# Kernel optimization log

Measured on AMD Instinct MI355X. Metric: run time of the kernel, lower is better.

## Reference

```python
import jax, jax.numpy as jnp
import numpy as np


def _pairwise_dist(x, y):
    # x: [b, n, d], y: [b, n, d] -> squared L2 distances [b, n, n]
    xx = jnp.sum(x * x, axis=-1)  # [b, n]
    yy = jnp.sum(y * y, axis=-1)  # [b, n]
    zz = jnp.einsum('bnd,bmd->bnm', x, y)  # [b, n, n]
    return xx[:, :, None] + yy[:, None, :] - 2.0 * zz


def setup_inputs() -> dict:
    key = jax.random.key(0)
    k1, k2 = jax.random.split(key)
    bs, n, d = 4, 8192, 3
    x = jax.random.normal(k1, (bs, n, d), dtype=jnp.float32)
    y = jax.random.normal(k2, (bs, n, d), dtype=jnp.float32)
    return {"x": x, "y": y}


def reference(x, y):
    bs, n_points, _ = x.shape
    dist1 = jnp.sqrt(_pairwise_dist(x, y))  # [b, n, n]
    values1 = jnp.min(dist1, axis=2)        # [b, n] min over y for each x point
    dist2 = jnp.sqrt(_pairwise_dist(y, x))
    values2 = jnp.min(dist2, axis=2)        # min over x for each y point
    a = jnp.sum(values1, axis=1) / n_points
    b = jnp.sum(values2, axis=1) / n_points
    return jnp.sum(a) / bs + jnp.sum(b) / bs
```

## Files before the change

kernel.cpp:

```cpp
#include <hip/hip_runtime.h>
#include <stdint.h>

typedef _Float16 half8 __attribute__((ext_vector_type(8)));
typedef float f32x16 __attribute__((ext_vector_type(16)));

#define NPTS 8192
#define BS 4
#define TOTQ 65536
#define TPB 256
#define NS 4
#define QPB 512
#define NCHUNK 4

#define AS1 __attribute__((address_space(1)))
#define AS3 __attribute__((address_space(3)))

__device__ __forceinline__ float4 f4min(float4 a, float4 b) {
    return make_float4(fminf(a.x, b.x), fminf(a.y, b.y), fminf(a.z, b.z), fminf(a.w, b.w));
}


__global__ __launch_bounds__(TPB) void pack_mfma_kernel(const float* __restrict__ x,
                                                        const float* __restrict__ y,
                                                        ushort* __restrict__ Afrag,
                                                        ushort* __restrict__ Bfrag,
                                                        float* __restrict__ nq) {
    int pid = blockIdx.x * TPB + threadIdx.x;
    const float* src = (pid < BS * NPTS) ? x : y;
    int idx = pid & (BS * NPTS - 1);
    float p0 = src[idx * 3 + 0], p1 = src[idx * 3 + 1], p2 = src[idx * 3 + 2];
    float nt = p0 * p0 + p1 * p1 + p2 * p2;

    _Float16 h0 = (_Float16)p0, h1 = (_Float16)p1, h2 = (_Float16)p2;
    _Float16 l0 = (_Float16)(p0 - (float)h0);
    _Float16 l1 = (_Float16)(p1 - (float)h1);
    _Float16 l2 = (_Float16)(p2 - (float)h2);
    _Float16 nh = (_Float16)nt;
    _Float16 nl = (_Float16)(nt - (float)nh);
    _Float16 t2 = (_Float16)-2.0f;
    _Float16 m0 = t2 * h0, m1 = t2 * h1, m2 = t2 * h2;
    _Float16 n0 = t2 * l0, n1 = t2 * l1, n2 = t2 * l2;
    _Float16 one = (_Float16)1.0f, zz = (_Float16)0.0f;

    half8 ag0 = {m0, m1, m2, n0, n1, n2, m0, m1};
    half8 ag1 = {m2, one, one, n0, n1, n2, zz, zz};
    half8 bg0 = {h0, h1, h2, h0, h1, h2, l0, l1};
    half8 bg1 = {l2, nh, nl, l0, l1, l2, zz, zz};

    int qid = pid;
    int tid2 = pid ^ (BS * NPTS);
    size_t ab = (size_t)(qid >> 5) * 512 + (size_t)(qid & 31) * 8;
    *(half8*)(Afrag + ab)       = ag0;
    *(half8*)(Afrag + ab + 256) = ag1;
    size_t bb = (size_t)(tid2 >> 5) * 512 + (size_t)(tid2 & 31) * 8;
    *(half8*)(Bfrag + bb)       = bg0;
    *(half8*)(Bfrag + bb + 256) = bg1;
    nq[qid] = nt;
}

__global__ __launch_bounds__(TPB, 2) void mfma_min_kernel(const ushort* __restrict__ Afrag,
                                                          const ushort* __restrict__ Bfrag,
                                                          float* __restrict__ partial) {
    __shared__ __align__(16) char lds[2][16384];
    const int tid = threadIdx.x;
    const int wave = tid >> 6;
    const int l = tid & 63;
    const int chunkid = blockIdx.x / NS;
    const int s = blockIdx.x % NS;
    const int qbase = chunkid * QPB;
    const int dir = qbase >> 15;
    const int b = (qbase >> 13) & 3;
    const int tbase = dir * (BS * NPTS) + b * NPTS + s * (NPTS / NS);

    half8 afr0, afr1, afr2, afr3;
    {
        const ushort* Aw = Afrag + ((size_t)(qbase >> 5) + wave * 4) * 512 + (size_t)l * 8;
        afr0 = *(const half8*)(Aw);
        afr1 = *(const half8*)(Aw + 512);
        afr2 = *(const half8*)(Aw + 1024);
        afr3 = *(const half8*)(Aw + 1536);
    }
    f32x16 mrun0, mrun1, mrun2, mrun3, zc;
#pragma unroll
    for (int r = 0; r < 16; ++r) {
        mrun0[r] = 3.4e38f; mrun1[r] = 3.4e38f;
        mrun2[r] = 3.4e38f; mrun3[r] = 3.4e38f;
        zc[r] = 0.0f;
    }

    const char* gB = (const char*)Bfrag + (size_t)(tbase >> 5) * 1024;

#define STAGE(buf, c)                                                                       \
    {                                                                                       \
        _Pragma("unroll")                                                                   \
        for (int i = 0; i < 4; ++i)                                                         \
            __builtin_amdgcn_global_load_lds(                                               \
                (const AS1 uint32_t*)(gB + (size_t)(c) * 16384 + i * 4096 + tid * 16),      \
                (AS3 uint32_t*)(&lds[buf][i * 4096 + wave * 1024]), 16, 0, 0);              \
    }

#define AGROUP(AF, MR, BB0, BB1)                                                            \
    {                                                                                       \
        f32x16 d0 = __builtin_amdgcn_mfma_f32_32x32x16_f16(AF, BB0, zc, 0, 0, 0);           \
        f32x16 d1 = __builtin_amdgcn_mfma_f32_32x32x16_f16(AF, BB1, zc, 0, 0, 0);           \
        _Pragma("unroll")                                                                   \
        for (int r = 0; r < 16; ++r)                                                        \
            MR[r] = fminf(fminf(MR[r], d0[r]), d1[r]);                                      \
        __builtin_amdgcn_sched_barrier(0);                                                  \
    }

#define COMPUTE(BB0, BB1)                                                                   \
    AGROUP(afr0, mrun0, BB0, BB1)                                                           \
    AGROUP(afr1, mrun1, BB0, BB1)                                                           \
    AGROUP(afr2, mrun2, BB0, BB1)                                                           \
    AGROUP(afr3, mrun3, BB0, BB1)

    STAGE(0, 0);
    __syncthreads();

    int cur = 0;
#pragma unroll 1
    for (int c = 0; c < NCHUNK; ++c) {
        if (c + 1 < NCHUNK) STAGE(cur ^ 1, c + 1);
        const char* B = lds[cur];
        half8 bA0 = *(const half8*)(B + l * 16);
        half8 bA1 = *(const half8*)(B + 1024 + l * 16);
        half8 bB0, bB1;
#pragma unroll 1
        for (int p = 0; p < 8; p += 2) {
            bB0 = *(const half8*)(B + (p + 1) * 2048 + l * 16);
            bB1 = *(const half8*)(B + (p + 1) * 2048 + 1024 + l * 16);
            COMPUTE(bA0, bA1);
            int pn = (p + 2) & 7;
            bA0 = *(const half8*)(B + pn * 2048 + l * 16);
            bA1 = *(const half8*)(B + pn * 2048 + 1024 + l * 16);
            COMPUTE(bB0, bB1);
        }
        if (c + 1 < NCHUNK) {
            __syncthreads();
            cur ^= 1;
        }
    }
#undef STAGE
#undef COMPUTE
#undef AGROUP

    __syncthreads();
    float* ep = (float*)(&lds[0][0]);
    const int hi4 = (l >> 5) * 4;
    const int col = l & 31;

#define EPASS(AA, MR)                                                                       \
    {                                                                                       \
        _Pragma("unroll")                                                                   \
        for (int r = 0; r < 16; ++r) {                                                      \
            int row = (r & 3) + 8 * (r >> 2) + hi4;                                         \
            ep[wave * 1152 + row * 36 + col] = MR[r];                                       \
        }                                                                                   \
    }                                                                                       \
    __syncthreads();                                                                        \
    if (tid < 128) {                                                                        \
        const float4* rp = (const float4*)(ep + (tid >> 5) * 1152 + (tid & 31) * 36);       \
        float4 a01 = f4min(rp[0], rp[1]), a23 = f4min(rp[2], rp[3]);                        \
        float4 a45 = f4min(rp[4], rp[5]), a67 = f4min(rp[6], rp[7]);                        \
        float4 t = f4min(f4min(a01, a23), f4min(a45, a67));                                 \
        float m = fminf(fminf(t.x, t.y), fminf(t.z, t.w));                                  \
        partial[(size_t)s * TOTQ + qbase + (tid >> 5) * 128 + (AA) * 32 + (tid & 31)] = m;  \
    }                                                                                       \
    __syncthreads();

    EPASS(0, mrun0)
    EPASS(1, mrun1)
    EPASS(2, mrun2)
    EPASS(3, mrun3)
#undef EPASS
}

__global__ __launch_bounds__(TPB) void combine_mfma_kernel(const float* __restrict__ partial,
                                                           const float* __restrict__ nq,
                                                           float* __restrict__ bsum) {
    int q = blockIdx.x * TPB + threadIdx.x;
    float m = partial[q];
#pragma unroll
    for (int s = 1; s < NS; ++s)
        m = fminf(m, partial[(size_t)s * TOTQ + q]);
    float d = sqrtf(fmaxf(m + nq[q], 0.0f));
    __shared__ float red[TPB];
    red[threadIdx.x] = d;
    __syncthreads();
    for (int off = TPB / 2; off > 0; off >>= 1) {
        if (threadIdx.x < off) red[threadIdx.x] += red[threadIdx.x + off];
        __syncthreads();
    }
    if (threadIdx.x == 0) bsum[blockIdx.x] = red[0];
}

__global__ __launch_bounds__(TPB) void final_kernel(const float* __restrict__ bsum,
                                                    float* __restrict__ out) {
    __shared__ float red[TPB];
    red[threadIdx.x] = bsum[threadIdx.x];
    __syncthreads();
    for (int off = TPB / 2; off > 0; off >>= 1) {
        if (threadIdx.x < off) red[threadIdx.x] += red[threadIdx.x + off];
        __syncthreads();
    }
    if (threadIdx.x == 0) out[0] = red[0] * (1.0f / 32768.0f);
}

#define QPT 8
#define QPBF (TPB * QPT)
#define NGROUP (TOTQ / QPBF)
#define FNS 8

__global__ __launch_bounds__(TPB) void pack_kernel(const float* __restrict__ x,
                                                   const float* __restrict__ y,
                                                   float4* __restrict__ px,
                                                   float4* __restrict__ py) {
    int i = blockIdx.x * TPB + threadIdx.x;
    if (i < BS * NPTS) {
        float x0 = x[i * 3 + 0], x1 = x[i * 3 + 1], x2 = x[i * 3 + 2];
        px[i] = make_float4(x0, x1, x2, x0 * x0 + x1 * x1 + x2 * x2);
        float y0 = y[i * 3 + 0], y1 = y[i * 3 + 1], y2 = y[i * 3 + 2];
        py[i] = make_float4(y0, y1, y2, y0 * y0 + y1 * y1 + y2 * y2);
    }
}

__global__ __launch_bounds__(TPB) void chamfer_min_kernel(const float4* __restrict__ px,
                                                          const float4* __restrict__ py,
                                                          float* __restrict__ partial) {
    constexpr int SLICE = NPTS / FNS;
    __shared__ float4 tile[SLICE];
    const int t = threadIdx.x;
    const int g = blockIdx.x / FNS;
    const int s = blockIdx.x % FNS;
    const int dir = g >> 4;
    const int b = (g >> 2) & 3;
    const int chunk = g & 3;
    const float4* q  = (dir == 0 ? px : py) + b * NPTS + chunk * QPBF;
    const float4* tg = (dir == 0 ? py : px) + b * NPTS + s * SLICE;
    float a0[QPT], a1[QPT], a2[QPT], qq[QPT], mv[QPT];
#pragma unroll
    for (int i = 0; i < QPT; ++i) {
        float4 v = q[i * TPB + t];
        a0[i] = -2.0f * v.x; a1[i] = -2.0f * v.y; a2[i] = -2.0f * v.z;
        qq[i] = v.w; mv[i] = 3.4e38f;
    }
#pragma unroll
    for (int i = 0; i < SLICE / TPB; ++i)
        tile[i * TPB + t] = tg[i * TPB + t];
    __syncthreads();
#pragma unroll 2
    for (int j = 0; j < SLICE; j += 2) {
        float4 v0 = tile[j], v1 = tile[j + 1];
#pragma unroll
        for (int i = 0; i < QPT; ++i) {
            float d0 = fmaf(a2[i], v0.z, fmaf(a1[i], v0.y, fmaf(a0[i], v0.x, v0.w)));
            float d1 = fmaf(a2[i], v1.z, fmaf(a1[i], v1.y, fmaf(a0[i], v1.x, v1.w)));
            mv[i] = fminf(fminf(mv[i], d0), d1);
        }
    }
    const int qg0 = g * QPBF;
#pragma unroll
    for (int i = 0; i < QPT; ++i)
        partial[(size_t)s * TOTQ + qg0 + i * TPB + t] = mv[i] + qq[i];
}

__global__ __launch_bounds__(TPB) void combine_kernel(const float* __restrict__ partial,
                                                      float* __restrict__ bsum) {
    int idx = blockIdx.x * TPB + threadIdx.x;
    float m = 3.4e38f;
#pragma unroll
    for (int s = 0; s < FNS; ++s)
        m = fminf(m, partial[(size_t)s * TOTQ + idx]);
    float d = sqrtf(fmaxf(m, 0.0f));
    __shared__ float red[TPB];
    red[threadIdx.x] = d;
    __syncthreads();
    for (int off = TPB / 2; off > 0; off >>= 1) {
        if (threadIdx.x < off) red[threadIdx.x] += red[threadIdx.x + off];
        __syncthreads();
    }
    if (threadIdx.x == 0) bsum[blockIdx.x] = red[0];
}

extern "C" void kernel_launch(void* const* d_in, const int* in_sizes, int n_in,
                              void* d_out, int out_size, void* d_ws, size_t ws_size,
                              hipStream_t stream) {
    const float* x = (const float*)d_in[0];
    const float* y = (const float*)d_in[1];
    float* out = (float*)d_out;
    char* ws = (char*)d_ws;

    const size_t off_B = 2ull << 20;
    const size_t off_nq = 4ull << 20;
    const size_t off_pt = off_nq + (size_t)TOTQ * 4;
    const size_t off_bs = off_pt + (size_t)NS * TOTQ * 4;
    const size_t need = off_bs + 1024;

    if (ws_size >= need) {
        ushort* Afrag = (ushort*)ws;
        ushort* Bfrag = (ushort*)(ws + off_B);
        float* nq = (float*)(ws + off_nq);
        float* partial = (float*)(ws + off_pt);
        float* bsum = (float*)(ws + off_bs);
        hipLaunchKernelGGL(pack_mfma_kernel, dim3(TOTQ / TPB), dim3(TPB), 0, stream,
                           x, y, Afrag, Bfrag, nq);
        hipLaunchKernelGGL(mfma_min_kernel, dim3((TOTQ / QPB) * NS), dim3(TPB), 0, stream,
                           Afrag, Bfrag, partial);
        hipLaunchKernelGGL(combine_mfma_kernel, dim3(TOTQ / TPB), dim3(TPB), 0, stream,
                           partial, nq, bsum);
        hipLaunchKernelGGL(final_kernel, dim3(1), dim3(TPB), 0, stream, bsum, out);
    } else {
        float4* px = (float4*)ws;
        float4* py = (float4*)(ws + 512 * 1024);
        float* partial = (float*)(ws + 1024 * 1024);
        float* bsum = (float*)(ws + 1024 * 1024 + (size_t)FNS * TOTQ * 4);
        hipLaunchKernelGGL(pack_kernel, dim3((BS * NPTS + TPB - 1) / TPB), dim3(TPB), 0, stream,
                           x, y, px, py);
        hipLaunchKernelGGL(chamfer_min_kernel, dim3(NGROUP * FNS), dim3(TPB), 0, stream,
                           px, py, partial);
        hipLaunchKernelGGL(combine_kernel, dim3(TOTQ / TPB), dim3(TPB), 0, stream,
                           partial, bsum);
        hipLaunchKernelGGL(final_kernel, dim3(1), dim3(TPB), 0, stream, bsum, out);
    }
}
```

Measured before the change: 33.72 us.

## Fuse final reduction via last-block atomic counter and software-pipeline MFMA/min folds

The final single-block reduction kernel is folded into the combine kernel. A global atomic counter, reset in the pack kernel, lets the last block to finish sum the per-block partials, which removes one kernel launch. The MFMA inner loop is also reordered so each pair of MFMAs for the next A fragment is issued before the fminf fold of the previous results, with sched barriers placed to overlap matrix work with VALU min work. This costs extra accumulator registers, which may reduce occupancy, and adds an atomic and a release/acquire ordering step to the combine path.

```diff
diff --git a/kernel.cpp b/kernel.cpp
--- a/kernel.cpp
+++ b/kernel.cpp
@@ -24,8 +24,10 @@
                                                         const float* __restrict__ y,
                                                         ushort* __restrict__ Afrag,
                                                         ushort* __restrict__ Bfrag,
-                                                        float* __restrict__ nq) {
+                                                        float* __restrict__ nq,
+                                                        int* __restrict__ counter) {
     int pid = blockIdx.x * TPB + threadIdx.x;
+    if (pid == 0) *counter = 0;
     const float* src = (pid < BS * NPTS) ? x : y;
     int idx = pid & (BS * NPTS - 1);
     float p0 = src[idx * 3 + 0], p1 = src[idx * 3 + 1], p2 = src[idx * 3 + 2];
@@ -99,21 +101,34 @@
                 (AS3 uint32_t*)(&lds[buf][i * 4096 + wave * 1024]), 16, 0, 0);              \
     }
 
-#define AGROUP(AF, MR, BB0, BB1)                                                            \
+#define PAIR(AF, D0, D1, BB0, BB1)                                                          \
+    D0 = __builtin_amdgcn_mfma_f32_32x32x16_f16(AF, BB0, zc, 0, 0, 0);                      \
+    D1 = __builtin_amdgcn_mfma_f32_32x32x16_f16(AF, BB1, zc, 0, 0, 0);
+
+#define FOLD(MR, D0, D1)                                                                    \
     {                                                                                       \
-        f32x16 d0 = __builtin_amdgcn_mfma_f32_32x32x16_f16(AF, BB0, zc, 0, 0, 0);           \
-        f32x16 d1 = __builtin_amdgcn_mfma_f32_32x32x16_f16(AF, BB1, zc, 0, 0, 0);           \
         _Pragma("unroll")                                                                   \
         for (int r = 0; r < 16; ++r)                                                        \
-            MR[r] = fminf(fminf(MR[r], d0[r]), d1[r]);                                      \
-        __builtin_amdgcn_sched_barrier(0);                                                  \
+            MR[r] = fminf(fminf(MR[r], D0[r]), D1[r]);                          \
     }
 
 #define COMPUTE(BB0, BB1)                                                                   \
-    AGROUP(afr0, mrun0, BB0, BB1)                                                           \
-    AGROUP(afr1, mrun1, BB0, BB1)                                                           \
-    AGROUP(afr2, mrun2, BB0, BB1)                                                           \
-    AGROUP(afr3, mrun3, BB0, BB1)
+    {                                                                                       \
+        f32x16 dP0, dP1, dQ0, dQ1;                                                          \
+        PAIR(afr0, dP0, dP1, BB0, BB1)                                                      \
+        __builtin_amdgcn_sched_barrier(0);                                                  \
+        PAIR(afr1, dQ0, dQ1, BB0, BB1)                                                      \
+        FOLD(mrun0, dP0, dP1)                                                               \
+        __builtin_amdgcn_sched_barrier(0);                                                  \
+        PAIR(afr2, dP0, dP1, BB0, BB1)                                                      \
+        FOLD(mrun1, dQ0, dQ1)                                                               \
+        __builtin_amdgcn_sched_barrier(0);                                                  \
+        PAIR(afr3, dQ0, dQ1, BB0, BB1)                                                      \
+        FOLD(mrun2, dP0, dP1)                                                               \
+        __builtin_amdgcn_sched_barrier(0);                                                  \
+        FOLD(mrun3, dQ0, dQ1)                                                               \
+        __builtin_amdgcn_sched_barrier(0);                                                  \
+    }
 
     STAGE(0, 0);
     __syncthreads();
@@ -143,7 +158,8 @@
     }
 #undef STAGE
 #undef COMPUTE
-#undef AGROUP
+#undef PAIR
+#undef FOLD
 
     __syncthreads();
     float* ep = (float*)(&lds[0][0]);
@@ -178,33 +194,43 @@
 
 __global__ __launch_bounds__(TPB) void combine_mfma_kernel(const float* __restrict__ partial,
                                                            const float* __restrict__ nq,
-                                                           float* __restrict__ bsum) {
+                                                           float* __restrict__ bsum,
+                                                           int* __restrict__ counter,
+                                                           float* __restrict__ out) {
     int q = blockIdx.x * TPB + threadIdx.x;
     float m = partial[q];
 #pragma unroll
     for (int s = 1; s < NS; ++s)
         m = fminf(m, partial[(size_t)s * TOTQ + q]);
     float d = sqrtf(fmaxf(m + nq[q], 0.0f));
+
     __shared__ float red[TPB];
+    __shared__ int islast;
     red[threadIdx.x] = d;
     __syncthreads();
     for (int off = TPB / 2; off > 0; off >>= 1) {
         if (threadIdx.x < off) red[threadIdx.x] += red[threadIdx.x + off];
         __syncthreads();
     }
-    if (threadIdx.x == 0) bsum[blockIdx.x] = red[0];
-}
-
-__global__ __launch_bounds__(TPB) void final_kernel(const float* __restrict__ bsum,
-                                                    float* __restrict__ out) {
-    __shared__ float red[TPB];
-    red[threadIdx.x] = bsum[threadIdx.x];
-    __syncthreads();
-    for (int off = TPB / 2; off > 0; off >>= 1) {
-        if (threadIdx.x < off) red[threadIdx.x] += red[threadIdx.x + off];
+    if (threadIdx.x == 0) {
+        __hip_atomic_store(&bsum[blockIdx.x], red[0], __ATOMIC_RELEASE,
+                           __HIP_MEMORY_SCOPE_AGENT);
+        int old = __hip_atomic_fetch_add(counter, 1, __ATOMIC_ACQ_REL,
+                                         __HIP_MEMORY_SCOPE_AGENT);
+        islast = (old == (int)gridDim.x - 1);
+    }
+    __syncthreads();
+    if (islast) {
+        float v = __hip_atomic_load(&bsum[threadIdx.x], __ATOMIC_ACQUIRE,
+                                    __HIP_MEMORY_SCOPE_AGENT);
+        red[threadIdx.x] = v;
         __syncthreads();
-    }
-    if (threadIdx.x == 0) out[0] = red[0] * (1.0f / 32768.0f);
+        for (int off = TPB / 2; off > 0; off >>= 1) {
+            if (threadIdx.x < off) red[threadIdx.x] += red[threadIdx.x + off];
+            __syncthreads();
+        }
+        if (threadIdx.x == 0) out[0] = red[0] * (1.0f / 32768.0f);
+    }
 }
 
 #define QPT 8
@@ -283,6 +309,18 @@
     if (threadIdx.x == 0) bsum[blockIdx.x] = red[0];
 }
 
+__global__ __launch_bounds__(TPB) void final_kernel(const float* __restrict__ bsum,
+                                                    float* __restrict__ out) {
+    __shared__ float red[TPB];
+    red[threadIdx.x] = bsum[threadIdx.x];
+    __syncthreads();
+    for (int off = TPB / 2; off > 0; off >>= 1) {
+        if (threadIdx.x < off) red[threadIdx.x] += red[threadIdx.x + off];
+        __syncthreads();
+    }
+    if (threadIdx.x == 0) out[0] = red[0] * (1.0f / 32768.0f);
+}
+
 extern "C" void kernel_launch(void* const* d_in, const int* in_sizes, int n_in,
                               void* d_out, int out_size, void* d_ws, size_t ws_size,
                               hipStream_t stream) {
@@ -295,7 +333,8 @@
     const size_t off_nq = 4ull << 20;
     const size_t off_pt = off_nq + (size_t)TOTQ * 4;
     const size_t off_bs = off_pt + (size_t)NS * TOTQ * 4;
-    const size_t need = off_bs + 1024;
+    const size_t off_cnt = off_bs + 1024;
+    const size_t need = off_cnt + 64;
 
     if (ws_size >= need) {
         ushort* Afrag = (ushort*)ws;
@@ -303,13 +342,13 @@
         float* nq = (float*)(ws + off_nq);
         float* partial = (float*)(ws + off_pt);
         float* bsum = (float*)(ws + off_bs);
+        int* counter = (int*)(ws + off_cnt);
         hipLaunchKernelGGL(pack_mfma_kernel, dim3(TOTQ / TPB), dim3(TPB), 0, stream,
-                           x, y, Afrag, Bfrag, nq);
+                           x, y, Afrag, Bfrag, nq, counter);
         hipLaunchKernelGGL(mfma_min_kernel, dim3((TOTQ / QPB) * NS), dim3(TPB), 0, stream,
                            Afrag, Bfrag, partial);
         hipLaunchKernelGGL(combine_mfma_kernel, dim3(TOTQ / TPB), dim3(TPB), 0, stream,
-                           partial, nq, bsum);
-        hipLaunchKernelGGL(final_kernel, dim3(1), dim3(TPB), 0, stream, bsum, out);
+                           partial, nq, bsum, counter, out);
     } else {
         float4* px = (float4*)ws;
         float4* py = (float4*)(ws + 512 * 1024);
```

Result: slower. 39.56 us (+17.3%).
